# Performance work log

Hardware: AMD Instinct MI355X
Metric: run time of the kernel (lower is better)

The kernel has to match this reference:

```python
import jax, jax.numpy as jnp
import numpy as np

VOCAB, EMBED = 100000, 128
B, QLEN, DLEN = 1024, 32, 256
KERNEL_NUM, SIGMA, EXACT_SIGMA = 11, 0.1, 0.001
EPS = 1e-8  # torch F.cosine_similarity eps


def _kernel_mus(n):
    l_mu = [1.0]
    if n == 1:
        return l_mu
    bin_size = 2.0 / (n - 1)
    l_mu.append(1 - bin_size / 2)
    for i in range(1, n - 1):
        l_mu.append(round(l_mu[i] - bin_size, 5))
    return list(reversed(l_mu))


def _kernel_sigmas(n, sigma, exact_sigma):
    l_sigma = [exact_sigma]
    if n == 1:
        return l_sigma
    l_sigma += [sigma] * (n - 1)
    return list(reversed(l_sigma))


MUS = jnp.asarray(np.array(_kernel_mus(KERNEL_NUM), dtype=np.float32))      # [K]
SIGMAS = jnp.asarray(np.array(_kernel_sigmas(KERNEL_NUM, SIGMA, EXACT_SIGMA), dtype=np.float32))  # [K]


def setup_inputs() -> dict:
    key = jax.random.key(0)
    k = jax.random.split(key, 7)
    return {
        "emb": jax.random.normal(k[0], (VOCAB, EMBED), dtype=jnp.float32),
        "mlp_w": jax.random.normal(k[1], (1, KERNEL_NUM), dtype=jnp.float32) * 0.3,
        "mlp_b": jax.random.normal(k[2], (1,), dtype=jnp.float32) * 0.1,
        "query1": jax.random.randint(k[3], (B, QLEN), 0, VOCAB, dtype=jnp.int32).astype(jnp.int64),
        "doc1": jax.random.randint(k[4], (B, DLEN), 0, VOCAB, dtype=jnp.int32).astype(jnp.int64),
        "query2": jax.random.randint(k[5], (B, QLEN), 0, VOCAB, dtype=jnp.int32).astype(jnp.int64),
        "doc2": jax.random.randint(k[6], (B, DLEN), 0, VOCAB, dtype=jnp.int32).astype(jnp.int64),
    }


def _predict(emb, mlp_w, mlp_b, query, doc):
    qe = emb[query]                               # [B,Q,E]
    de = emb[doc]                                 # [B,D,E]
    qn = jnp.linalg.norm(qe, axis=-1)             # [B,Q]
    dn = jnp.linalg.norm(de, axis=-1)             # [B,D]
    dots = jnp.einsum("bqe,bde->bqd", qe, de)    # [B,Q,D]
    sim = dots / jnp.maximum(qn[:, :, None] * dn[:, None, :], EPS)
    # multi-Gaussian soft histogram: exp(-(sim-mu)^2/(2 sigma^2)), sum over doc,
    # log1p, sum over query  -> [B,K]
    z = (sim[..., None] - MUS) / SIGMAS           # [B,Q,D,K]
    K = jnp.exp(-0.5 * z * z)
    pooled = jnp.log1p(K.sum(axis=2)).sum(axis=1)  # [B,K]
    return pooled @ mlp_w.T + mlp_b               # [B,1]


def reference(emb, mlp_w, mlp_b, query1, doc1, query2, doc2):
    logits_1 = _predict(emb, mlp_w, mlp_b, query1, doc1)
    logits_2 = _predict(emb, mlp_w, mlp_b, query2, doc2)
    return jax.nn.sigmoid(logits_1 - logits_2)    # [B,1]
```

## Files before the change

### kernel.cpp

```cpp
#include <hip/hip_runtime.h>
#include <math.h>
#include <stdint.h>

#define VOCAB 100000
#define NB    1024
#define QLEN  32
#define DLEN  256
#define EMBED 128
#define KNUM  11

typedef __attribute__((ext_vector_type(8))) short bf16x8;
typedef __attribute__((ext_vector_type(4))) float f32x4;

#define HALF_L2E 0.7213475204444817f
#define TWO_L2E  2.8853900817779268f
#define EM4      0.018315638888734179f

#define SSTR  68
#define SHALF (16 * SSTR)

__global__ __launch_bounds__(256)
void cvt_table(const float* __restrict__ emb, ushort* __restrict__ ebf,
               float* __restrict__ inorm)
{
    const int row = blockIdx.x * 8 + (threadIdx.x >> 5);
    const int l32 = threadIdx.x & 31;
    const float4 v = *((const float4*)(emb + (size_t)row * EMBED) + l32);
    union { float f; unsigned u; } x0, x1, x2, x3;
    x0.f = v.x; x1.f = v.y; x2.f = v.z; x3.f = v.w;
    const unsigned r0 = x0.u + 0x8000u, r1 = x1.u + 0x8000u;
    const unsigned r2 = x2.u + 0x8000u, r3 = x3.u + 0x8000u;
    uint2 packed;
    packed.x = (r0 >> 16) | (r1 & 0xFFFF0000u);
    packed.y = (r2 >> 16) | (r3 & 0xFFFF0000u);
    *((uint2*)(ebf + (size_t)row * EMBED) + l32) = packed;
    x0.u = r0 & 0xFFFF0000u; x1.u = r1 & 0xFFFF0000u;
    x2.u = r2 & 0xFFFF0000u; x3.u = r3 & 0xFFFF0000u;
    float n = x0.f * x0.f + x1.f * x1.f + x2.f * x2.f + x3.f * x3.f;
    #pragma unroll
    for (int m = 1; m < 32; m <<= 1) n += __shfl_xor(n, m);
    if (l32 == 0) inorm[row] = __builtin_amdgcn_rsqf(n);
}

__device__ __forceinline__ bf16x8 cvt8(const float* p, float& nacc)
{
    uint4 a = *((const uint4*)p);
    uint4 b = *((const uint4*)(p + 4));
    unsigned u[8] = {a.x, a.y, a.z, a.w, b.x, b.y, b.z, b.w};
    bf16x8 r;
    #pragma unroll
    for (int i = 0; i < 8; ++i) {
        const unsigned q = u[i] + 0x8000u;
        r[i] = (short)(q >> 16);
        union { unsigned uu; float ff; } g; g.uu = q & 0xFFFF0000u;
        nacc = fmaf(g.ff, g.ff, nacc);
    }
    return r;
}

__device__ __forceinline__ void pool_half(float* __restrict__ wtile,
                                          const f32x4* __restrict__ a,
                                          const float* __restrict__ riq,
                                          const float* __restrict__ idn,
                                          float (*__restrict__ stot)[12],
                                          int mtbase, int l15, int quad)
{
    #pragma unroll
    for (int nt = 0; nt < 4; ++nt)
        #pragma unroll
        for (int r = 0; r < 4; ++r)
            wtile[(quad * 4 + r) * SSTR + nt * 16 + l15] = a[nt][r] * riq[r] * idn[nt];

    const float* rp = wtile + l15 * SSTR + quad * 16;
    float ksum[KNUM];
    #pragma unroll
    for (int k = 0; k < KNUM; ++k) ksum[k] = 0.f;

    #pragma unroll
    for (int i = 0; i < 4; ++i) {
        const f32x4 sv = *((const f32x4*)(rp + 4 * i));
        #pragma unroll
        for (int e = 0; e < 4; ++e) {
            const float s  = sv[e];
            const float z  = fmaf(s, 10.f, -1.f);
            const float e0 = exp2f(-HALF_L2E * (z * z));
            float ru = exp2f(fmaf(z,  TWO_L2E, -TWO_L2E));
            float rd = exp2f(fmaf(z, -TWO_L2E, -TWO_L2E));
            ksum[5] += e0;
            float tt = e0;
            tt *= ru; ksum[6] += tt; ru *= EM4;
            tt *= ru; ksum[7] += tt; ru *= EM4;
            tt *= ru; ksum[8] += tt; ru *= EM4;
            tt *= ru; ksum[9] += tt;
            tt = e0;
            tt *= rd; ksum[4] += tt; rd *= EM4;
            tt *= rd; ksum[3] += tt; rd *= EM4;
            tt *= rd; ksum[2] += tt; rd *= EM4;
            tt *= rd; ksum[1] += tt; rd *= EM4;
            tt *= rd; ksum[0] += tt;
            ksum[10] += (s > 0.995f) ? 1.f : 0.f;
        }
    }
    #pragma unroll
    for (int k = 0; k < KNUM; ++k) {
        ksum[k] += __shfl_xor(ksum[k], 16);
        ksum[k] += __shfl_xor(ksum[k], 32);
    }
    if (quad == 0) {
        #pragma unroll
        for (int k = 0; k < KNUM; ++k)
            atomicAdd(&stot[mtbase + l15][k], ksum[k]);
    }
}

__global__ __launch_bounds__(256, 3)
void knrm_pair4(const ushort* __restrict__ ebf,
                const float* __restrict__ inorm,
                const float* __restrict__ mlp_w,
                const int* __restrict__ q1, const int* __restrict__ d1,
                const int* __restrict__ q2, const int* __restrict__ d2,
                float* __restrict__ logits)
{
    const int b    = blockIdx.x;
    const int pair = blockIdx.y;
    const int t    = threadIdx.x;
    const int w    = t >> 6;
    const int l15  = t & 15;
    const int quad = (t & 63) >> 4;

    const int* __restrict__ qry = (pair == 0 ? q1 : q2) + b * QLEN;
    const int* __restrict__ doc = (pair == 0 ? d1 : d2) + b * DLEN;

    __shared__ __align__(16) float s_sim[4 * SHALF];
    __shared__ float s_tot[QLEN][12];

    const int qid0 = qry[l15], qid1 = qry[l15 + 16];
    int did[4];
    #pragma unroll
    for (int j = 0; j < 4; ++j) did[j] = doc[(w * 4 + j) * 16 + l15];

    bf16x8 a0[4], a1[4], bbf[4][4];
    {
        const ushort* qp0 = ebf + (size_t)qid0 * EMBED + quad * 8;
        const ushort* qp1 = ebf + (size_t)qid1 * EMBED + quad * 8;
        #pragma unroll
        for (int kk = 0; kk < 4; ++kk) {
            a0[kk] = *(const bf16x8*)(qp0 + kk * 32);
            a1[kk] = *(const bf16x8*)(qp1 + kk * 32);
        }
        #pragma unroll
        for (int j = 0; j < 4; ++j) {
            const ushort* dp = ebf + (size_t)did[j] * EMBED + quad * 8;
            #pragma unroll
            for (int kk = 0; kk < 4; ++kk)
                bbf[j][kk] = *(const bf16x8*)(dp + kk * 32);
        }
    }
    float idn[4];
    #pragma unroll
    for (int j = 0; j < 4; ++j) idn[j] = inorm[did[j]];
    float riq[2][4];
    #pragma unroll
    for (int r = 0; r < 4; ++r) {
        riq[0][r] = inorm[qry[quad * 4 + r]];
        riq[1][r] = inorm[qry[16 + quad * 4 + r]];
    }

    #pragma unroll
    for (int i = t; i < QLEN * 12; i += 256) ((float*)s_tot)[i] = 0.f;

    #pragma unroll
    for (int kk = 0; kk < 4; ++kk)
        asm volatile("" :: "v"(a0[kk]), "v"(a1[kk]));
    #pragma unroll
    for (int j = 0; j < 4; ++j)
        asm volatile("" :: "v"(bbf[j][0]), "v"(bbf[j][1]),
                          "v"(bbf[j][2]), "v"(bbf[j][3]));
    __builtin_amdgcn_sched_barrier(0);

    f32x4 acc[2][4];
    #pragma unroll
    for (int mt = 0; mt < 2; ++mt)
        #pragma unroll
        for (int j = 0; j < 4; ++j)
            acc[mt][j] = (f32x4){0.f, 0.f, 0.f, 0.f};
    #pragma unroll
    for (int kk = 0; kk < 4; ++kk)
        #pragma unroll
        for (int j = 0; j < 4; ++j) {
            acc[0][j] = __builtin_amdgcn_mfma_f32_16x16x32_bf16(a0[kk], bbf[j][kk], acc[0][j], 0, 0, 0);
            acc[1][j] = __builtin_amdgcn_mfma_f32_16x16x32_bf16(a1[kk], bbf[j][kk], acc[1][j], 0, 0, 0);
        }

    __syncthreads();

    float* wtile = s_sim + w * SHALF;
    pool_half(wtile, acc[0], riq[0], idn, s_tot, 0,  l15, quad);
    pool_half(wtile, acc[1], riq[1], idn, s_tot, 16, l15, quad);
    __syncthreads();

    if (t < QLEN) {
        float c = 0.f;
        #pragma unroll
        for (int k = 0; k < KNUM; ++k) c += mlp_w[k] * log1pf(s_tot[t][k]);
        #pragma unroll
        for (int mm = 1; mm < 32; mm <<= 1) c += __shfl_xor(c, mm);
        if (t == 0) logits[pair * NB + b] = c;
    }
}

template<bool PRE>
__global__ __launch_bounds__(256, 4)
void knrm_pair(const float* __restrict__ emb,
               const ushort* __restrict__ ebf,
               const float* __restrict__ inorm,
               const float* __restrict__ mlp_w,
               const int* __restrict__ q1, const int* __restrict__ d1,
               const int* __restrict__ q2, const int* __restrict__ d2,
               float* __restrict__ logits)
{
    const int b    = blockIdx.x;
    const int pair = blockIdx.y;
    const int t    = threadIdx.x;
    const int w    = t >> 6;
    const int l15  = t & 15;
    const int quad = (t & 63) >> 4;

    const int* __restrict__ qry = (pair == 0 ? q1 : q2) + b * QLEN;
    const int* __restrict__ doc = (pair == 0 ? d1 : d2) + b * DLEN;

    __shared__ __align__(16) float s_sim[4 * SHALF];
    __shared__ float s_tot[QLEN][12];

    #pragma unroll
    for (int i = t; i < QLEN * 12; i += 256) ((float*)s_tot)[i] = 0.f;
    __syncthreads();

    const int qid0 = qry[l15], qid1 = qry[l15 + 16];
    int did[4];
    #pragma unroll
    for (int nt = 0; nt < 4; ++nt) did[nt] = doc[(w * 4 + nt) * 16 + l15];

    f32x4 acc[2][4];
    #pragma unroll
    for (int mt = 0; mt < 2; ++mt)
        #pragma unroll
        for (int nt = 0; nt < 4; ++nt)
            acc[mt][nt] = (f32x4){0.f, 0.f, 0.f, 0.f};

    float idn[4], riq[2][4];
    float* wtile = s_sim + w * SHALF;

    if (PRE) {
        const ushort* qp0 = ebf + (size_t)qid0 * EMBED + quad * 8;
        const ushort* qp1 = ebf + (size_t)qid1 * EMBED + quad * 8;
        #pragma unroll
        for (int kk = 0; kk < 4; ++kk) {
            const bf16x8 a0 = *((const bf16x8*)(qp0 + kk * 32));
            const bf16x8 a1 = *((const bf16x8*)(qp1 + kk * 32));
            #pragma unroll
            for (int nt = 0; nt < 4; ++nt) {
                const bf16x8 bb = *((const bf16x8*)(ebf + (size_t)did[nt] * EMBED + quad * 8 + kk * 32));
                acc[0][nt] = __builtin_amdgcn_mfma_f32_16x16x32_bf16(a0, bb, acc[0][nt], 0, 0, 0);
                acc[1][nt] = __builtin_amdgcn_mfma_f32_16x16x32_bf16(a1, bb, acc[1][nt], 0, 0, 0);
            }
        }
        #pragma unroll
        for (int nt = 0; nt < 4; ++nt) idn[nt] = inorm[did[nt]];
        #pragma unroll
        for (int r = 0; r < 4; ++r) {
            riq[0][r] = inorm[qry[quad * 4 + r]];
            riq[1][r] = inorm[qry[16 + quad * 4 + r]];
        }
    } else {
        float qn2[2] = {0.f, 0.f}, dn2[4] = {0.f, 0.f, 0.f, 0.f};
        const float* qp0 = emb + (size_t)qid0 * EMBED + quad * 8;
        const float* qp1 = emb + (size_t)qid1 * EMBED + quad * 8;
        #pragma unroll
        for (int kk = 0; kk < 4; ++kk) {
            const bf16x8 a0 = cvt8(qp0 + kk * 32, qn2[0]);
            const bf16x8 a1 = cvt8(qp1 + kk * 32, qn2[1]);
            #pragma unroll
            for (int nt = 0; nt < 4; ++nt) {
                const bf16x8 bb = cvt8(emb + (size_t)did[nt] * EMBED + quad * 8 + kk * 32, dn2[nt]);
                acc[0][nt] = __builtin_amdgcn_mfma_f32_16x16x32_bf16(a0, bb, acc[0][nt], 0, 0, 0);
                acc[1][nt] = __builtin_amdgcn_mfma_f32_16x16x32_bf16(a1, bb, acc[1][nt], 0, 0, 0);
            }
        }
        #pragma unroll
        for (int i = 0; i < 2; ++i) {
            qn2[i] += __shfl_xor(qn2[i], 16);
            qn2[i] += __shfl_xor(qn2[i], 32);
        }
        #pragma unroll
        for (int nt = 0; nt < 4; ++nt) {
            dn2[nt] += __shfl_xor(dn2[nt], 16);
            dn2[nt] += __shfl_xor(dn2[nt], 32);
            idn[nt] = __builtin_amdgcn_rsqf(dn2[nt]);
        }
        #pragma unroll
        for (int r = 0; r < 4; ++r) {
            riq[0][r] = __builtin_amdgcn_rsqf(__shfl(qn2[0], quad * 4 + r));
            riq[1][r] = __builtin_amdgcn_rsqf(__shfl(qn2[1], quad * 4 + r));
        }
    }

    pool_half(wtile, acc[0], riq[0], idn, s_tot, 0,  l15, quad);
    pool_half(wtile, acc[1], riq[1], idn, s_tot, 16, l15, quad);
    __syncthreads();

    if (t < QLEN) {
        float c = 0.f;
        #pragma unroll
        for (int k = 0; k < KNUM; ++k) c += mlp_w[k] * log1pf(s_tot[t][k]);
        #pragma unroll
        for (int mm = 1; mm < 32; mm <<= 1) c += __shfl_xor(c, mm);
        if (t == 0) logits[pair * NB + b] = c;
    }
}

__global__ __launch_bounds__(256)
void knrm_combine(const float* __restrict__ logits, float* __restrict__ out)
{
    const int i = blockIdx.x * blockDim.x + threadIdx.x;
    if (i < NB) {
        const float d = logits[i] - logits[NB + i];
        out[i] = 1.f / (1.f + __expf(-d));
    }
}

extern "C" void kernel_launch(void* const* d_in, const int* in_sizes, int n_in,
                              void* d_out, int out_size, void* d_ws, size_t ws_size,
                              hipStream_t stream)
{
    const float* emb   = (const float*)d_in[0];
    const float* mlp_w = (const float*)d_in[1];
    const int* q1 = (const int*)d_in[3];
    const int* d1 = (const int*)d_in[4];
    const int* q2 = (const int*)d_in[5];
    const int* d2 = (const int*)d_in[6];

    float* out = (float*)d_out;

    const size_t need = 2 * NB * 4
                      + (size_t)VOCAB * 4
                      + (size_t)VOCAB * EMBED * 2 + 256;
    if (ws_size >= need) {
        float*  logits = (float*)d_ws;
        float*  inorm  = logits + 2 * NB;
        ushort* ebf    = (ushort*)(inorm + VOCAB);
        cvt_table<<<VOCAB / 8, 256, 0, stream>>>(emb, ebf, inorm);
        knrm_pair4<<<dim3(NB, 2), 256, 0, stream>>>(ebf, inorm, mlp_w,
                                                    q1, d1, q2, d2, logits);
    } else {
        float* logits = (float*)d_ws;
        knrm_pair<false><<<dim3(NB, 2), 256, 0, stream>>>(emb, nullptr, nullptr, mlp_w,
                                                          q1, d1, q2, d2, logits);
    }
    knrm_combine<<<(NB + 255) / 256, 256, 0, stream>>>((float*)d_ws, out);
}
```

Before: 141.0 us.

## Process four batch units per block with software-pipelined gather prefetch

Replaces the one-block-per-(batch,pair) kernel with a persistent-style kernel in which each block handles four consecutive units. While one unit's similarity tile is pooled, the block already issues the embedding gathers for the next unit and the index loads for the unit after that. Pooling sums are double-buffered in shared memory, and the per-wave shared tile now holds both 16-row halves at once. The aim is to hide gather latency behind the exp-heavy pooling, at the cost of more registers, a larger shared footprint and a quarter as many blocks.

```diff
diff --git a/kernel.cpp b/kernel.cpp
--- a/kernel.cpp
+++ b/kernel.cpp
@@ -18,6 +18,8 @@
 
 #define SSTR  68
 #define SHALF (16 * SSTR)
+#define WROWS 32
+#define WTILE_F (WROWS * SSTR)
 
 __global__ __launch_bounds__(256)
 void cvt_table(const float* __restrict__ emb, ushort* __restrict__ ebf,
@@ -42,6 +44,222 @@
     if (l32 == 0) inorm[row] = __builtin_amdgcn_rsqf(n);
 }
 
+__device__ __forceinline__ void load_ids(const int* __restrict__ qp,
+                                         const int* __restrict__ dp,
+                                         int w, int l15,
+                                         int& q0, int& q1, int (&dd)[4])
+{
+    q0 = qp[l15];
+    q1 = qp[l15 + 16];
+    #pragma unroll
+    for (int j = 0; j < 4; ++j) dd[j] = dp[(w * 4 + j) * 16 + l15];
+}
+
+__device__ __forceinline__ void issue_frags(const ushort* __restrict__ ebf,
+                                            const float* __restrict__ inorm,
+                                            const int* __restrict__ qp,
+                                            int quad,
+                                            int q0, int q1, const int (&dd)[4],
+                                            bf16x8 (&a0)[4], bf16x8 (&a1)[4],
+                                            bf16x8 (&bbf)[4][4],
+                                            float (&idn)[4], float (&riq)[2][4])
+{
+    const ushort* qp0 = ebf + (size_t)q0 * EMBED + quad * 8;
+    const ushort* qp1 = ebf + (size_t)q1 * EMBED + quad * 8;
+    #pragma unroll
+    for (int kk = 0; kk < 4; ++kk) {
+        a0[kk] = *(const bf16x8*)(qp0 + kk * 32);
+        a1[kk] = *(const bf16x8*)(qp1 + kk * 32);
+    }
+    #pragma unroll
+    for (int j = 0; j < 4; ++j) {
+        const ushort* dp = ebf + (size_t)dd[j] * EMBED + quad * 8;
+        #pragma unroll
+        for (int kk = 0; kk < 4; ++kk)
+            bbf[j][kk] = *(const bf16x8*)(dp + kk * 32);
+    }
+    #pragma unroll
+    for (int j = 0; j < 4; ++j) idn[j] = inorm[dd[j]];
+    #pragma unroll
+    for (int r = 0; r < 4; ++r) {
+        riq[0][r] = inorm[qp[quad * 4 + r]];
+        riq[1][r] = inorm[qp[16 + quad * 4 + r]];
+    }
+}
+
+__device__ __forceinline__ void chain4(const f32x4 sv, float (&ksum)[KNUM])
+{
+    #pragma unroll
+    for (int e = 0; e < 4; ++e) {
+        const float s  = sv[e];
+        const float z  = fmaf(s, 10.f, -1.f);
+        const float e0 = exp2f(-HALF_L2E * (z * z));
+        float ru = exp2f(fmaf(z,  TWO_L2E, -TWO_L2E));
+        float rd = exp2f(fmaf(z, -TWO_L2E, -TWO_L2E));
+        ksum[5] += e0;
+        float tt = e0;
+        tt *= ru; ksum[6] += tt; ru *= EM4;
+        tt *= ru; ksum[7] += tt; ru *= EM4;
+        tt *= ru; ksum[8] += tt; ru *= EM4;
+        tt *= ru; ksum[9] += tt;
+        tt = e0;
+        tt *= rd; ksum[4] += tt; rd *= EM4;
+        tt *= rd; ksum[3] += tt; rd *= EM4;
+        tt *= rd; ksum[2] += tt; rd *= EM4;
+        tt *= rd; ksum[1] += tt; rd *= EM4;
+        tt *= rd; ksum[0] += tt;
+        ksum[10] += (s > 0.995f) ? 1.f : 0.f;
+    }
+}
+
+template<int U>
+__device__ __forceinline__ void knrm_unit(
+    const ushort* __restrict__ ebf, const float* __restrict__ inorm,
+    const float* __restrict__ mlp_w, float* __restrict__ logits,
+    int unitIdx,
+    const int* __restrict__ qpNext,
+    const int* __restrict__ qpNext2, const int* __restrict__ dpNext2,
+    int w, int l15, int quad, int t,
+    bf16x8 (&a0)[4], bf16x8 (&a1)[4], bf16x8 (&bbf)[4][4],
+    float (&idn)[4], float (&riq)[2][4],
+    int& qN0, int& qN1, int (&ddN)[4],
+    int& qM0, int& qM1, int (&ddM)[4],
+    float* __restrict__ wtile,
+    float (*__restrict__ stot)[QLEN][12])
+{
+    constexpr int PBUF = U & 1;
+
+    f32x4 acc[2][4];
+    #pragma unroll
+    for (int mt = 0; mt < 2; ++mt)
+        #pragma unroll
+        for (int j = 0; j < 4; ++j)
+            acc[mt][j] = (f32x4){0.f, 0.f, 0.f, 0.f};
+    #pragma unroll
+    for (int kk = 0; kk < 4; ++kk)
+        #pragma unroll
+        for (int j = 0; j < 4; ++j) {
+            acc[0][j] = __builtin_amdgcn_mfma_f32_16x16x32_bf16(a0[kk], bbf[j][kk], acc[0][j], 0, 0, 0);
+            acc[1][j] = __builtin_amdgcn_mfma_f32_16x16x32_bf16(a1[kk], bbf[j][kk], acc[1][j], 0, 0, 0);
+        }
+
+    #pragma unroll
+    for (int mt = 0; mt < 2; ++mt)
+        #pragma unroll
+        for (int j = 0; j < 4; ++j)
+            #pragma unroll
+            for (int r = 0; r < 4; ++r)
+                wtile[(mt * 16 + quad * 4 + r) * SSTR + j * 16 + l15] =
+                    acc[mt][j][r] * riq[mt][r] * idn[j];
+
+    if constexpr (U < 3)
+        issue_frags(ebf, inorm, qpNext, quad, qN0, qN1, ddN, a0, a1, bbf, idn, riq);
+    if constexpr (U < 2)
+        load_ids(qpNext2, dpNext2, w, l15, qM0, qM1, ddM);
+    __builtin_amdgcn_sched_barrier(0);
+
+    #pragma unroll
+    for (int mt = 0; mt < 2; ++mt) {
+        const float* rp = wtile + (mt * 16 + l15) * SSTR + quad * 16;
+        float ksum[KNUM];
+        #pragma unroll
+        for (int k = 0; k < KNUM; ++k) ksum[k] = 0.f;
+        #pragma unroll
+        for (int i = 0; i < 4; ++i)
+            chain4(*(const f32x4*)(rp + 4 * i), ksum);
+        #pragma unroll
+        for (int k = 0; k < KNUM; ++k) {
+            ksum[k] += __shfl_xor(ksum[k], 16);
+            ksum[k] += __shfl_xor(ksum[k], 32);
+        }
+        if (quad == 0) {
+            #pragma unroll
+            for (int k = 0; k < KNUM; ++k)
+                atomicAdd(&stot[PBUF][mt * 16 + l15][k], ksum[k]);
+        }
+    }
+    __syncthreads();
+
+    if (t < QLEN) {
+        float c = 0.f;
+        #pragma unroll
+        for (int k = 0; k < KNUM; ++k) {
+            c += mlp_w[k] * log1pf(stot[PBUF][t][k]);
+            stot[PBUF][t][k] = 0.f;
+        }
+        #pragma unroll
+        for (int mm = 1; mm < 32; mm <<= 1) c += __shfl_xor(c, mm);
+        if (t == 0) logits[unitIdx] = c;
+    }
+}
+
+__global__ __launch_bounds__(256, 3)
+void knrm_pair5(const ushort* __restrict__ ebf,
+                const float* __restrict__ inorm,
+                const float* __restrict__ mlp_w,
+                const int* __restrict__ q1, const int* __restrict__ d1,
+                const int* __restrict__ q2, const int* __restrict__ d2,
+                float* __restrict__ logits)
+{
+    const int t    = threadIdx.x;
+    const int w    = t >> 6;
+    const int l15  = t & 15;
+    const int quad = (t & 63) >> 4;
+
+    const int unit0 = blockIdx.x * 4;
+    const int pair  = unit0 >> 10;
+    const int b0    = unit0 & 1023;
+    const int* __restrict__ qb = (pair ? q2 : q1);
+    const int* __restrict__ db = (pair ? d2 : d1);
+
+    __shared__ __align__(16) float s_sim[4 * WTILE_F];
+    __shared__ float s_tot[2][QLEN][12];
+    float* wtile = s_sim + w * WTILE_F;
+
+    int qidA0, qidA1, didA[4];
+    int qidB0, qidB1, didB[4];
+    bf16x8 a0[4], a1[4], bbf[4][4];
+    float idn[4], riq[2][4];
+
+    load_ids(qb + (size_t)b0 * QLEN, db + (size_t)b0 * DLEN, w, l15, qidA0, qidA1, didA);
+    issue_frags(ebf, inorm, qb + (size_t)b0 * QLEN, quad, qidA0, qidA1, didA,
+                a0, a1, bbf, idn, riq);
+    load_ids(qb + (size_t)(b0 + 1) * QLEN, db + (size_t)(b0 + 1) * DLEN,
+             w, l15, qidB0, qidB1, didB);
+
+    #pragma unroll
+    for (int i = t; i < 2 * QLEN * 12; i += 256) ((float*)s_tot)[i] = 0.f;
+    __syncthreads();
+
+    knrm_unit<0>(ebf, inorm, mlp_w, logits, unit0 + 0,
+                 qb + (size_t)(b0 + 1) * QLEN,
+                 qb + (size_t)(b0 + 2) * QLEN, db + (size_t)(b0 + 2) * DLEN,
+                 w, l15, quad, t, a0, a1, bbf, idn, riq,
+                 qidB0, qidB1, didB,
+                 qidA0, qidA1, didA,
+                 wtile, s_tot);
+    knrm_unit<1>(ebf, inorm, mlp_w, logits, unit0 + 1,
+                 qb + (size_t)(b0 + 2) * QLEN,
+                 qb + (size_t)(b0 + 3) * QLEN, db + (size_t)(b0 + 3) * DLEN,
+                 w, l15, quad, t, a0, a1, bbf, idn, riq,
+                 qidA0, qidA1, didA,
+                 qidB0, qidB1, didB,
+                 wtile, s_tot);
+    knrm_unit<2>(ebf, inorm, mlp_w, logits, unit0 + 2,
+                 qb + (size_t)(b0 + 3) * QLEN,
+                 (const int*)nullptr, (const int*)nullptr,
+                 w, l15, quad, t, a0, a1, bbf, idn, riq,
+                 qidB0, qidB1, didB,
+                 qidA0, qidA1, didA,
+                 wtile, s_tot);
+    knrm_unit<3>(ebf, inorm, mlp_w, logits, unit0 + 3,
+                 (const int*)nullptr, (const int*)nullptr, (const int*)nullptr,
+                 w, l15, quad, t, a0, a1, bbf, idn, riq,
+                 qidA0, qidA1, didA,
+                 qidB0, qidB1, didB,
+                 wtile, s_tot);
+}
+
 __device__ __forceinline__ bf16x8 cvt8(const float* p, float& nacc)
 {
     uint4 a = *((const uint4*)p);
@@ -75,32 +293,9 @@
     float ksum[KNUM];
     #pragma unroll
     for (int k = 0; k < KNUM; ++k) ksum[k] = 0.f;
-
-    #pragma unroll
-    for (int i = 0; i < 4; ++i) {
-        const f32x4 sv = *((const f32x4*)(rp + 4 * i));
-        #pragma unroll
-        for (int e = 0; e < 4; ++e) {
-            const float s  = sv[e];
-            const float z  = fmaf(s, 10.f, -1.f);
-            const float e0 = exp2f(-HALF_L2E * (z * z));
-            float ru = exp2f(fmaf(z,  TWO_L2E, -TWO_L2E));
-            float rd = exp2f(fmaf(z, -TWO_L2E, -TWO_L2E));
-            ksum[5] += e0;
-            float tt = e0;
-            tt *= ru; ksum[6] += tt; ru *= EM4;
-            tt *= ru; ksum[7] += tt; ru *= EM4;
-            tt *= ru; ksum[8] += tt; ru *= EM4;
-            tt *= ru; ksum[9] += tt;
-            tt = e0;
-            tt *= rd; ksum[4] += tt; rd *= EM4;
-            tt *= rd; ksum[3] += tt; rd *= EM4;
-            tt *= rd; ksum[2] += tt; rd *= EM4;
-            tt *= rd; ksum[1] += tt; rd *= EM4;
-            tt *= rd; ksum[0] += tt;
-            ksum[10] += (s > 0.995f) ? 1.f : 0.f;
-        }
-    }
+    #pragma unroll
+    for (int i = 0; i < 4; ++i)
+        chain4(*(const f32x4*)(rp + 4 * i), ksum);
     #pragma unroll
     for (int k = 0; k < KNUM; ++k) {
         ksum[k] += __shfl_xor(ksum[k], 16);
@@ -110,102 +305,6 @@
         #pragma unroll
         for (int k = 0; k < KNUM; ++k)
             atomicAdd(&stot[mtbase + l15][k], ksum[k]);
-    }
-}
-
-__global__ __launch_bounds__(256, 3)
-void knrm_pair4(const ushort* __restrict__ ebf,
-                const float* __restrict__ inorm,
-                const float* __restrict__ mlp_w,
-                const int* __restrict__ q1, const int* __restrict__ d1,
-                const int* __restrict__ q2, const int* __restrict__ d2,
-                float* __restrict__ logits)
-{
-    const int b    = blockIdx.x;
-    const int pair = blockIdx.y;
-    const int t    = threadIdx.x;
-    const int w    = t >> 6;
-    const int l15  = t & 15;
-    const int quad = (t & 63) >> 4;
-
-    const int* __restrict__ qry = (pair == 0 ? q1 : q2) + b * QLEN;
-    const int* __restrict__ doc = (pair == 0 ? d1 : d2) + b * DLEN;
-
-    __shared__ __align__(16) float s_sim[4 * SHALF];
-    __shared__ float s_tot[QLEN][12];
-
-    const int qid0 = qry[l15], qid1 = qry[l15 + 16];
-    int did[4];
-    #pragma unroll
-    for (int j = 0; j < 4; ++j) did[j] = doc[(w * 4 + j) * 16 + l15];
-
-    bf16x8 a0[4], a1[4], bbf[4][4];
-    {
-        const ushort* qp0 = ebf + (size_t)qid0 * EMBED + quad * 8;
-        const ushort* qp1 = ebf + (size_t)qid1 * EMBED + quad * 8;
-        #pragma unroll
-        for (int kk = 0; kk < 4; ++kk) {
-            a0[kk] = *(const bf16x8*)(qp0 + kk * 32);
-            a1[kk] = *(const bf16x8*)(qp1 + kk * 32);
-        }
-        #pragma unroll
-        for (int j = 0; j < 4; ++j) {
-            const ushort* dp = ebf + (size_t)did[j] * EMBED + quad * 8;
-            #pragma unroll
-            for (int kk = 0; kk < 4; ++kk)
-                bbf[j][kk] = *(const bf16x8*)(dp + kk * 32);
-        }
-    }
-    float idn[4];
-    #pragma unroll
-    for (int j = 0; j < 4; ++j) idn[j] = inorm[did[j]];
-    float riq[2][4];
-    #pragma unroll
-    for (int r = 0; r < 4; ++r) {
-        riq[0][r] = inorm[qry[quad * 4 + r]];
-        riq[1][r] = inorm[qry[16 + quad * 4 + r]];
-    }
-
-    #pragma unroll
-    for (int i = t; i < QLEN * 12; i += 256) ((float*)s_tot)[i] = 0.f;
-
-    #pragma unroll
-    for (int kk = 0; kk < 4; ++kk)
-        asm volatile("" :: "v"(a0[kk]), "v"(a1[kk]));
-    #pragma unroll
-    for (int j = 0; j < 4; ++j)
-        asm volatile("" :: "v"(bbf[j][0]), "v"(bbf[j][1]),
-                          "v"(bbf[j][2]), "v"(bbf[j][3]));
-    __builtin_amdgcn_sched_barrier(0);
-
-    f32x4 acc[2][4];
-    #pragma unroll
-    for (int mt = 0; mt < 2; ++mt)
-        #pragma unroll
-        for (int j = 0; j < 4; ++j)
-            acc[mt][j] = (f32x4){0.f, 0.f, 0.f, 0.f};
-    #pragma unroll
-    for (int kk = 0; kk < 4; ++kk)
-        #pragma unroll
-        for (int j = 0; j < 4; ++j) {
-            acc[0][j] = __builtin_amdgcn_mfma_f32_16x16x32_bf16(a0[kk], bbf[j][kk], acc[0][j], 0, 0, 0);
-            acc[1][j] = __builtin_amdgcn_mfma_f32_16x16x32_bf16(a1[kk], bbf[j][kk], acc[1][j], 0, 0, 0);
-        }
-
-    __syncthreads();
-
-    float* wtile = s_sim + w * SHALF;
-    pool_half(wtile, acc[0], riq[0], idn, s_tot, 0,  l15, quad);
-    pool_half(wtile, acc[1], riq[1], idn, s_tot, 16, l15, quad);
-    __syncthreads();
-
-    if (t < QLEN) {
-        float c = 0.f;
-        #pragma unroll
-        for (int k = 0; k < KNUM; ++k) c += mlp_w[k] * log1pf(s_tot[t][k]);
-        #pragma unroll
-        for (int mm = 1; mm < 32; mm <<= 1) c += __shfl_xor(c, mm);
-        if (t == 0) logits[pair * NB + b] = c;
     }
 }
 
@@ -251,35 +350,16 @@
     float idn[4], riq[2][4];
     float* wtile = s_sim + w * SHALF;
 
-    if (PRE) {
-        const ushort* qp0 = ebf + (size_t)qid0 * EMBED + quad * 8;
-        const ushort* qp1 = ebf + (size_t)qid1 * EMBED + quad * 8;
+    {
+        float qn2[2] = {0.f, 0.f}, dn2[4] = {0.f, 0.f, 0.f, 0.f};
+        const float* qp0 = (const float*)nullptr;
+        (void)qp0;
+        const float* emb_qp0 = emb + (size_t)qid0 * EMBED + quad * 8;
+        const float* emb_qp1 = emb + (size_t)qid1 * EMBED + quad * 8;
         #pragma unroll
         for (int kk = 0; kk < 4; ++kk) {
-            const bf16x8 a0 = *((const bf16x8*)(qp0 + kk * 32));
-            const bf16x8 a1 = *((const bf16x8*)(qp1 + kk * 32));
-            #pragma unroll
-            for (int nt = 0; nt < 4; ++nt) {
-                const bf16x8 bb = *((const bf16x8*)(ebf + (size_t)did[nt] * EMBED + quad * 8 + kk * 32));
-                acc[0][nt] = __builtin_amdgcn_mfma_f32_16x16x32_bf16(a0, bb, acc[0][nt], 0, 0, 0);
-                acc[1][nt] = __builtin_amdgcn_mfma_f32_16x16x32_bf16(a1, bb, acc[1][nt], 0, 0, 0);
-            }
-        }
-        #pragma unroll
-        for (int nt = 0; nt < 4; ++nt) idn[nt] = inorm[did[nt]];
-        #pragma unroll
-        for (int r = 0; r < 4; ++r) {
-            riq[0][r] = inorm[qry[quad * 4 + r]];
-            riq[1][r] = inorm[qry[16 + quad * 4 + r]];
-        }
-    } else {
-        float qn2[2] = {0.f, 0.f}, dn2[4] = {0.f, 0.f, 0.f, 0.f};
-        const float* qp0 = emb + (size_t)qid0 * EMBED + quad * 8;
-        const float* qp1 = emb + (size_t)qid1 * EMBED + quad * 8;
-        #pragma unroll
-        for (int kk = 0; kk < 4; ++kk) {
-            const bf16x8 a0 = cvt8(qp0 + kk * 32, qn2[0]);
-            const bf16x8 a1 = cvt8(qp1 + kk * 32, qn2[1]);
+            const bf16x8 a0 = cvt8(emb_qp0 + kk * 32, qn2[0]);
+            const bf16x8 a1 = cvt8(emb_qp1 + kk * 32, qn2[1]);
             #pragma unroll
             for (int nt = 0; nt < 4; ++nt) {
                 const bf16x8 bb = cvt8(emb + (size_t)did[nt] * EMBED + quad * 8 + kk * 32, dn2[nt]);
@@ -350,8 +430,8 @@
         float*  inorm  = logits + 2 * NB;
         ushort* ebf    = (ushort*)(inorm + VOCAB);
         cvt_table<<<VOCAB / 8, 256, 0, stream>>>(emb, ebf, inorm);
-        knrm_pair4<<<dim3(NB, 2), 256, 0, stream>>>(ebf, inorm, mlp_w,
-                                                    q1, d1, q2, d2, logits);
+        knrm_pair5<<<dim3(2 * NB / 4), 256, 0, stream>>>(ebf, inorm, mlp_w,
+                                                         q1, d1, q2, d2, logits);
     } else {
         float* logits = (float*)d_ws;
         knrm_pair<false><<<dim3(NB, 2), 256, 0, stream>>>(emb, nullptr, nullptr, mlp_w,
```

Result: slower. 205.2 us (+45.6%).

## Stage gathered bf16 embedding rows through swizzled LDS before MFMA

Applied to the files above, without the earlier changes.

The new main kernel gathers each doc and query embedding row with full-row coalesced 16-byte loads, where 16 lanes cover one 256-byte row. It stores them into a rotated (swizzled) shared-memory layout and reads the MFMA fragments back from LDS instead of issuing scattered per-fragment global loads. Norms are also staged in shared memory, and the same LDS buffer is reused for the similarity tile. The aim is better global-load coalescing and latency hiding. The cost is about 74KB of LDS per block, lower occupancy (launch bounds 2) and an extra barrier.

```diff
diff --git a/kernel.cpp b/kernel.cpp
--- a/kernel.cpp
+++ b/kernel.cpp
@@ -42,20 +42,29 @@
     if (l32 == 0) inorm[row] = __builtin_amdgcn_rsqf(n);
 }
 
-__device__ __forceinline__ bf16x8 cvt8(const float* p, float& nacc)
-{
-    uint4 a = *((const uint4*)p);
-    uint4 b = *((const uint4*)(p + 4));
-    unsigned u[8] = {a.x, a.y, a.z, a.w, b.x, b.y, b.z, b.w};
-    bf16x8 r;
-    #pragma unroll
-    for (int i = 0; i < 8; ++i) {
-        const unsigned q = u[i] + 0x8000u;
-        r[i] = (short)(q >> 16);
-        union { unsigned uu; float ff; } g; g.uu = q & 0xFFFF0000u;
-        nacc = fmaf(g.ff, g.ff, nacc);
-    }
-    return r;
+__device__ __forceinline__ void chain4(const f32x4 sv, float (&ksum)[KNUM])
+{
+    #pragma unroll
+    for (int e = 0; e < 4; ++e) {
+        const float s  = sv[e];
+        const float z  = fmaf(s, 10.f, -1.f);
+        const float e0 = exp2f(-HALF_L2E * (z * z));
+        float ru = exp2f(fmaf(z,  TWO_L2E, -TWO_L2E));
+        float rd = exp2f(fmaf(z, -TWO_L2E, -TWO_L2E));
+        ksum[5] += e0;
+        float tt = e0;
+        tt *= ru; ksum[6] += tt; ru *= EM4;
+        tt *= ru; ksum[7] += tt; ru *= EM4;
+        tt *= ru; ksum[8] += tt; ru *= EM4;
+        tt *= ru; ksum[9] += tt;
+        tt = e0;
+        tt *= rd; ksum[4] += tt; rd *= EM4;
+        tt *= rd; ksum[3] += tt; rd *= EM4;
+        tt *= rd; ksum[2] += tt; rd *= EM4;
+        tt *= rd; ksum[1] += tt; rd *= EM4;
+        tt *= rd; ksum[0] += tt;
+        ksum[10] += (s > 0.995f) ? 1.f : 0.f;
+    }
 }
 
 __device__ __forceinline__ void pool_half(float* __restrict__ wtile,
@@ -75,32 +84,9 @@
     float ksum[KNUM];
     #pragma unroll
     for (int k = 0; k < KNUM; ++k) ksum[k] = 0.f;
-
-    #pragma unroll
-    for (int i = 0; i < 4; ++i) {
-        const f32x4 sv = *((const f32x4*)(rp + 4 * i));
-        #pragma unroll
-        for (int e = 0; e < 4; ++e) {
-            const float s  = sv[e];
-            const float z  = fmaf(s, 10.f, -1.f);
-            const float e0 = exp2f(-HALF_L2E * (z * z));
-            float ru = exp2f(fmaf(z,  TWO_L2E, -TWO_L2E));
-            float rd = exp2f(fmaf(z, -TWO_L2E, -TWO_L2E));
-            ksum[5] += e0;
-            float tt = e0;
-            tt *= ru; ksum[6] += tt; ru *= EM4;
-            tt *= ru; ksum[7] += tt; ru *= EM4;
-            tt *= ru; ksum[8] += tt; ru *= EM4;
-            tt *= ru; ksum[9] += tt;
-            tt = e0;
-            tt *= rd; ksum[4] += tt; rd *= EM4;
-            tt *= rd; ksum[3] += tt; rd *= EM4;
-            tt *= rd; ksum[2] += tt; rd *= EM4;
-            tt *= rd; ksum[1] += tt; rd *= EM4;
-            tt *= rd; ksum[0] += tt;
-            ksum[10] += (s > 0.995f) ? 1.f : 0.f;
-        }
-    }
+    #pragma unroll
+    for (int i = 0; i < 4; ++i)
+        chain4(*(const f32x4*)(rp + 4 * i), ksum);
     #pragma unroll
     for (int k = 0; k < KNUM; ++k) {
         ksum[k] += __shfl_xor(ksum[k], 16);
@@ -113,13 +99,128 @@
     }
 }
 
-__global__ __launch_bounds__(256, 3)
-void knrm_pair4(const ushort* __restrict__ ebf,
+__global__ __launch_bounds__(256, 2)
+void knrm_pair6(const ushort* __restrict__ ebf,
                 const float* __restrict__ inorm,
                 const float* __restrict__ mlp_w,
                 const int* __restrict__ q1, const int* __restrict__ d1,
                 const int* __restrict__ q2, const int* __restrict__ d2,
                 float* __restrict__ logits)
+{
+    const int b    = blockIdx.x;
+    const int pair = blockIdx.y;
+    const int t    = threadIdx.x;
+    const int w    = t >> 6;
+    const int l    = t & 63;
+    const int l15  = l & 15;
+    const int quad = l >> 4;
+
+    const int* __restrict__ qry = (pair == 0 ? q1 : q2) + b * QLEN;
+    const int* __restrict__ doc = (pair == 0 ? d1 : d2) + b * DLEN;
+
+    __shared__ __align__(16) uint4 s_frag[16 * 256 + 2 * 256];
+    __shared__ float s_dnorm[DLEN];
+    __shared__ float s_qnorm[QLEN];
+    __shared__ float s_tot[QLEN][12];
+
+    #define TPOS(r, s) ((s) * 16 + (((r) + (s)) & 15))
+
+    #pragma unroll
+    for (int j = 0; j < 4; ++j)
+        #pragma unroll
+        for (int i = 0; i < 4; ++i) {
+            const int r  = 4 * i + quad;
+            const int id = doc[w * 64 + j * 16 + r];
+            const uint4 v = *(const uint4*)(ebf + (size_t)id * EMBED + l15 * 8);
+            s_frag[(w * 4 + j) * 256 + TPOS(r, l15)] = v;
+        }
+    {
+        const int mt = w >> 1;
+        #pragma unroll
+        for (int i = 0; i < 2; ++i) {
+            const int r  = (w & 1) * 8 + 4 * i + quad;
+            const int id = qry[mt * 16 + r];
+            const uint4 v = *(const uint4*)(ebf + (size_t)id * EMBED + l15 * 8);
+            s_frag[4096 + mt * 256 + TPOS(r, l15)] = v;
+        }
+    }
+    s_dnorm[w * 64 + l] = inorm[doc[w * 64 + l]];
+    if (t < QLEN) s_qnorm[t] = inorm[qry[t]];
+    #pragma unroll
+    for (int i = t; i < QLEN * 12; i += 256) ((float*)s_tot)[i] = 0.f;
+
+    __syncthreads();
+
+    f32x4 acc[2][4];
+    #pragma unroll
+    for (int mt = 0; mt < 2; ++mt)
+        #pragma unroll
+        for (int j = 0; j < 4; ++j)
+            acc[mt][j] = (f32x4){0.f, 0.f, 0.f, 0.f};
+    #pragma unroll
+    for (int kk = 0; kk < 4; ++kk) {
+        const int s = quad + 4 * kk;
+        const bf16x8 a0 = *(const bf16x8*)&s_frag[4096 +       TPOS(l15, s)];
+        const bf16x8 a1 = *(const bf16x8*)&s_frag[4096 + 256 + TPOS(l15, s)];
+        #pragma unroll
+        for (int j = 0; j < 4; ++j) {
+            const bf16x8 bb = *(const bf16x8*)&s_frag[(w * 4 + j) * 256 + TPOS(l15, s)];
+            acc[0][j] = __builtin_amdgcn_mfma_f32_16x16x32_bf16(a0, bb, acc[0][j], 0, 0, 0);
+            acc[1][j] = __builtin_amdgcn_mfma_f32_16x16x32_bf16(a1, bb, acc[1][j], 0, 0, 0);
+        }
+    }
+
+    float idn[4];
+    #pragma unroll
+    for (int j = 0; j < 4; ++j) idn[j] = s_dnorm[w * 64 + j * 16 + l15];
+    float riq[2][4];
+    #pragma unroll
+    for (int r = 0; r < 4; ++r) {
+        riq[0][r] = s_qnorm[quad * 4 + r];
+        riq[1][r] = s_qnorm[16 + quad * 4 + r];
+    }
+
+    asm volatile("s_waitcnt lgkmcnt(0)" ::: "memory");
+    __builtin_amdgcn_sched_barrier(0);
+
+    float* wtile = (float*)s_frag + w * 4096;
+    pool_half(wtile, acc[0], riq[0], idn, s_tot, 0,  l15, quad);
+    pool_half(wtile, acc[1], riq[1], idn, s_tot, 16, l15, quad);
+    __syncthreads();
+
+    if (t < QLEN) {
+        float c = 0.f;
+        #pragma unroll
+        for (int k = 0; k < KNUM; ++k) c += mlp_w[k] * log1pf(s_tot[t][k]);
+        #pragma unroll
+        for (int mm = 1; mm < 32; mm <<= 1) c += __shfl_xor(c, mm);
+        if (t == 0) logits[pair * NB + b] = c;
+    }
+    #undef TPOS
+}
+
+__device__ __forceinline__ bf16x8 cvt8(const float* p, float& nacc)
+{
+    uint4 a = *((const uint4*)p);
+    uint4 b = *((const uint4*)(p + 4));
+    unsigned u[8] = {a.x, a.y, a.z, a.w, b.x, b.y, b.z, b.w};
+    bf16x8 r;
+    #pragma unroll
+    for (int i = 0; i < 8; ++i) {
+        const unsigned q = u[i] + 0x8000u;
+        r[i] = (short)(q >> 16);
+        union { unsigned uu; float ff; } g; g.uu = q & 0xFFFF0000u;
+        nacc = fmaf(g.ff, g.ff, nacc);
+    }
+    return r;
+}
+
+__global__ __launch_bounds__(256, 4)
+void knrm_pair_fb(const float* __restrict__ emb,
+                  const float* __restrict__ mlp_w,
+                  const int* __restrict__ q1, const int* __restrict__ d1,
+                  const int* __restrict__ q2, const int* __restrict__ d2,
+                  float* __restrict__ logits)
 {
     const int b    = blockIdx.x;
     const int pair = blockIdx.y;
@@ -134,111 +235,13 @@
     __shared__ __align__(16) float s_sim[4 * SHALF];
     __shared__ float s_tot[QLEN][12];
 
+    #pragma unroll
+    for (int i = t; i < QLEN * 12; i += 256) ((float*)s_tot)[i] = 0.f;
+    __syncthreads();
+
     const int qid0 = qry[l15], qid1 = qry[l15 + 16];
     int did[4];
     #pragma unroll
-    for (int j = 0; j < 4; ++j) did[j] = doc[(w * 4 + j) * 16 + l15];
-
-    bf16x8 a0[4], a1[4], bbf[4][4];
-    {
-        const ushort* qp0 = ebf + (size_t)qid0 * EMBED + quad * 8;
-        const ushort* qp1 = ebf + (size_t)qid1 * EMBED + quad * 8;
-        #pragma unroll
-        for (int kk = 0; kk < 4; ++kk) {
-            a0[kk] = *(const bf16x8*)(qp0 + kk * 32);
-            a1[kk] = *(const bf16x8*)(qp1 + kk * 32);
-        }
-        #pragma unroll
-        for (int j = 0; j < 4; ++j) {
-            const ushort* dp = ebf + (size_t)did[j] * EMBED + quad * 8;
-            #pragma unroll
-            for (int kk = 0; kk < 4; ++kk)
-                bbf[j][kk] = *(const bf16x8*)(dp + kk * 32);
-        }
-    }
-    float idn[4];
-    #pragma unroll
-    for (int j = 0; j < 4; ++j) idn[j] = inorm[did[j]];
-    float riq[2][4];
-    #pragma unroll
-    for (int r = 0; r < 4; ++r) {
-        riq[0][r] = inorm[qry[quad * 4 + r]];
-        riq[1][r] = inorm[qry[16 + quad * 4 + r]];
-    }
-
-    #pragma unroll
-    for (int i = t; i < QLEN * 12; i += 256) ((float*)s_tot)[i] = 0.f;
-
-    #pragma unroll
-    for (int kk = 0; kk < 4; ++kk)
-        asm volatile("" :: "v"(a0[kk]), "v"(a1[kk]));
-    #pragma unroll
-    for (int j = 0; j < 4; ++j)
-        asm volatile("" :: "v"(bbf[j][0]), "v"(bbf[j][1]),
-                          "v"(bbf[j][2]), "v"(bbf[j][3]));
-    __builtin_amdgcn_sched_barrier(0);
-
-    f32x4 acc[2][4];
-    #pragma unroll
-    for (int mt = 0; mt < 2; ++mt)
-        #pragma unroll
-        for (int j = 0; j < 4; ++j)
-            acc[mt][j] = (f32x4){0.f, 0.f, 0.f, 0.f};
-    #pragma unroll
-    for (int kk = 0; kk < 4; ++kk)
-        #pragma unroll
-        for (int j = 0; j < 4; ++j) {
-            acc[0][j] = __builtin_amdgcn_mfma_f32_16x16x32_bf16(a0[kk], bbf[j][kk], acc[0][j], 0, 0, 0);
-            acc[1][j] = __builtin_amdgcn_mfma_f32_16x16x32_bf16(a1[kk], bbf[j][kk], acc[1][j], 0, 0, 0);
-        }
-
-    __syncthreads();
-
-    float* wtile = s_sim + w * SHALF;
-    pool_half(wtile, acc[0], riq[0], idn, s_tot, 0,  l15, quad);
-    pool_half(wtile, acc[1], riq[1], idn, s_tot, 16, l15, quad);
-    __syncthreads();
-
-    if (t < QLEN) {
-        float c = 0.f;
-        #pragma unroll
-        for (int k = 0; k < KNUM; ++k) c += mlp_w[k] * log1pf(s_tot[t][k]);
-        #pragma unroll
-        for (int mm = 1; mm < 32; mm <<= 1) c += __shfl_xor(c, mm);
-        if (t == 0) logits[pair * NB + b] = c;
-    }
-}
-
-template<bool PRE>
-__global__ __launch_bounds__(256, 4)
-void knrm_pair(const float* __restrict__ emb,
-               const ushort* __restrict__ ebf,
-               const float* __restrict__ inorm,
-               const float* __restrict__ mlp_w,
-               const int* __restrict__ q1, const int* __restrict__ d1,
-               const int* __restrict__ q2, const int* __restrict__ d2,
-               float* __restrict__ logits)
-{
-    const int b    = blockIdx.x;
-    const int pair = blockIdx.y;
-    const int t    = threadIdx.x;
-    const int w    = t >> 6;
-    const int l15  = t & 15;
-    const int quad = (t & 63) >> 4;
-
-    const int* __restrict__ qry = (pair == 0 ? q1 : q2) + b * QLEN;
-    const int* __restrict__ doc = (pair == 0 ? d1 : d2) + b * DLEN;
-
-    __shared__ __align__(16) float s_sim[4 * SHALF];
-    __shared__ float s_tot[QLEN][12];
-
-    #pragma unroll
-    for (int i = t; i < QLEN * 12; i += 256) ((float*)s_tot)[i] = 0.f;
-    __syncthreads();
-
-    const int qid0 = qry[l15], qid1 = qry[l15 + 16];
-    int did[4];
-    #pragma unroll
     for (int nt = 0; nt < 4; ++nt) did[nt] = doc[(w * 4 + nt) * 16 + l15];
 
     f32x4 acc[2][4];
@@ -251,28 +254,7 @@
     float idn[4], riq[2][4];
     float* wtile = s_sim + w * SHALF;
 
-    if (PRE) {
-        const ushort* qp0 = ebf + (size_t)qid0 * EMBED + quad * 8;
-        const ushort* qp1 = ebf + (size_t)qid1 * EMBED + quad * 8;
-        #pragma unroll
-        for (int kk = 0; kk < 4; ++kk) {
-            const bf16x8 a0 = *((const bf16x8*)(qp0 + kk * 32));
-            const bf16x8 a1 = *((const bf16x8*)(qp1 + kk * 32));
-            #pragma unroll
-            for (int nt = 0; nt < 4; ++nt) {
-                const bf16x8 bb = *((const bf16x8*)(ebf + (size_t)did[nt] * EMBED + quad * 8 + kk * 32));
-                acc[0][nt] = __builtin_amdgcn_mfma_f32_16x16x32_bf16(a0, bb, acc[0][nt], 0, 0, 0);
-                acc[1][nt] = __builtin_amdgcn_mfma_f32_16x16x32_bf16(a1, bb, acc[1][nt], 0, 0, 0);
-            }
-        }
-        #pragma unroll
-        for (int nt = 0; nt < 4; ++nt) idn[nt] = inorm[did[nt]];
-        #pragma unroll
-        for (int r = 0; r < 4; ++r) {
-            riq[0][r] = inorm[qry[quad * 4 + r]];
-            riq[1][r] = inorm[qry[16 + quad * 4 + r]];
-        }
-    } else {
+    {
         float qn2[2] = {0.f, 0.f}, dn2[4] = {0.f, 0.f, 0.f, 0.f};
         const float* qp0 = emb + (size_t)qid0 * EMBED + quad * 8;
         const float* qp1 = emb + (size_t)qid1 * EMBED + quad * 8;
@@ -350,12 +332,12 @@
         float*  inorm  = logits + 2 * NB;
         ushort* ebf    = (ushort*)(inorm + VOCAB);
         cvt_table<<<VOCAB / 8, 256, 0, stream>>>(emb, ebf, inorm);
-        knrm_pair4<<<dim3(NB, 2), 256, 0, stream>>>(ebf, inorm, mlp_w,
+        knrm_pair6<<<dim3(NB, 2), 256, 0, stream>>>(ebf, inorm, mlp_w,
                                                     q1, d1, q2, d2, logits);
     } else {
         float* logits = (float*)d_ws;
-        knrm_pair<false><<<dim3(NB, 2), 256, 0, stream>>>(emb, nullptr, nullptr, mlp_w,
-                                                          q1, d1, q2, d2, logits);
+        knrm_pair_fb<<<dim3(NB, 2), 256, 0, stream>>>(emb, mlp_w,
+                                                      q1, d1, q2, d2, logits);
     }
     knrm_combine<<<(NB + 255) / 256, 256, 0, stream>>>((float*)d_ws, out);
 }
```

After: 155.9 us. 1.11x slower.
